# Kernel tuning notes

Measured on AMD Instinct MI355X. Metric: run time of the kernel, lower is better.

## Reference

```python
import jax, jax.numpy as jnp
import numpy as np

JACCARD_THRESH = 0.5
NEGPOS_RATIO = 3
VAR = (0.1, 0.2)


def point_form(p):
    # center-size (cx,cy,w,h) -> corner (xmin,ymin,xmax,ymax)
    return jnp.concatenate([p[:, :2] - p[:, 2:] / 2, p[:, :2] + p[:, 2:] / 2], axis=1)


def jaccard(a, b):
    # a: [No,4] corner boxes, b: [Np,4] corner boxes -> IoU [No,Np]
    lt = jnp.maximum(a[:, None, :2], b[None, :, :2])
    rb = jnp.minimum(a[:, None, 2:], b[None, :, 2:])
    wh = jnp.clip(rb - lt, 0.0)
    inter = wh[..., 0] * wh[..., 1]
    area_a = ((a[:, 2] - a[:, 0]) * (a[:, 3] - a[:, 1]))[:, None]
    area_b = ((b[:, 2] - b[:, 0]) * (b[:, 3] - b[:, 1]))[None, :]
    return inter / (area_a + area_b - inter)


def encode(matched, priors):
    # matched: [Np,4] corner GT, priors: [Np,4] center-size
    g_cxcy = ((matched[:, :2] + matched[:, 2:]) / 2 - priors[:, :2]) / (VAR[0] * priors[:, 2:])
    g_wh = jnp.log((matched[:, 2:] - matched[:, :2]) / priors[:, 2:]) / VAR[1]
    return jnp.concatenate([g_cxcy, g_wh], axis=1)


def match_one(truths, labels, priors):
    # truths: [No,4], labels: [No], priors: [Np,4] center-size
    overlaps = jaccard(truths, point_form(priors))          # [No,Np]
    best_prior_idx = jnp.argmax(overlaps, axis=1)           # [No]
    best_truth_overlap = jnp.max(overlaps, axis=0)          # [Np]
    best_truth_idx = jnp.argmax(overlaps, axis=0)           # [Np]
    # each GT keeps its best prior (overlap forced to 2)
    best_truth_overlap = best_truth_overlap.at[best_prior_idx].set(2.0)
    best_truth_idx = best_truth_idx.at[best_prior_idx].set(jnp.arange(truths.shape[0]))
    matched = truths[best_truth_idx]                        # [Np,4]
    conf = labels[best_truth_idx].astype(jnp.int32) + 1     # background = 0
    conf = jnp.where(best_truth_overlap < JACCARD_THRESH, 0, conf)
    return encode(matched, priors), conf


def reference(loc_data, conf_data, dbox_list, targets):
    num_batch, num_dbox, num_classes = conf_data.shape
    truths = targets[:, :, :4]
    labels = targets[:, :, 4]
    loc_t, conf_t = jax.vmap(match_one, in_axes=(0, 0, None))(truths, labels, dbox_list)
    pos_mask = conf_t > 0                                   # [B,Np]
    # localization loss: SmoothL1 (beta=1), summed over positive dboxes
    diff = loc_data - loc_t
    ad = jnp.abs(diff)
    sl1 = jnp.where(ad < 1.0, 0.5 * diff * diff, ad - 0.5)
    loss_l = jnp.sum(sl1 * pos_mask[..., None].astype(sl1.dtype))
    # per-dbox cross entropy
    logp = jax.nn.log_softmax(conf_data, axis=-1)
    ce = -jnp.take_along_axis(logp, conf_t[..., None], axis=-1)[..., 0]  # [B,Np]
    # hard negative mining: rank (descending) of pos-zeroed CE via double argsort
    loss_c_hnm = jnp.where(pos_mask, 0.0, ce)
    loss_idx = jnp.argsort(-loss_c_hnm, axis=1)
    idx_rank = jnp.argsort(loss_idx, axis=1)
    num_pos = jnp.sum(pos_mask, axis=1, keepdims=True)      # [B,1]
    num_neg = jnp.minimum(num_pos * NEGPOS_RATIO, num_dbox)
    neg_mask = idx_rank < num_neg
    sel = jnp.logical_or(pos_mask, neg_mask)
    loss_c = jnp.sum(jnp.where(sel, ce, 0.0))
    N = jnp.sum(num_pos).astype(loss_l.dtype)
    return loss_l / N, loss_c / N


def setup_inputs() -> dict:
    key = jax.random.key(0)
    ks = jax.random.split(key, 7)
    B, Np, C, No = 128, 8732, 21, 16
    loc_data = jax.random.normal(ks[0], (B, Np, 4), dtype=jnp.float32) * 0.1
    conf_data = jax.random.normal(ks[1], (B, Np, C), dtype=jnp.float32)
    # default boxes in center-size form, w/h strictly positive
    cxcy = jax.random.uniform(ks[2], (Np, 2), minval=0.05, maxval=0.95)
    wh = jax.random.uniform(ks[3], (Np, 2), minval=0.05, maxval=0.5)
    dbox_list = jnp.concatenate([cxcy, wh], axis=1).astype(jnp.float32)
    # ground truth: valid corner-form boxes + class label in [0,20)
    gcxcy = jax.random.uniform(ks[4], (B, No, 2), minval=0.2, maxval=0.8)
    gwh = jax.random.uniform(ks[5], (B, No, 2), minval=0.05, maxval=0.3)
    boxes = jnp.concatenate([gcxcy - gwh / 2, gcxcy + gwh / 2], axis=-1)
    lab = jax.random.randint(ks[6], (B, No, 1), 0, C - 1).astype(jnp.float32)
    targets = jnp.concatenate([boxes, lab], axis=-1).astype(jnp.float32)
    return {"loc_data": loc_data, "conf_data": conf_data, "dbox_list": dbox_list, "targets": targets}
```

## Files before the change

kernel.cpp:

```cpp
#include <hip/hip_runtime.h>
#include <stdint.h>

#define TPB 256
#define PPT 4
#define SELTPB 1024
#define SELWAVES (SELTPB / 64)
#define MAXNO 64
#define NMB 16

__device__ __forceinline__ float sl1f(float d) {
    float ad = fabsf(d);
    return ad < 1.0f ? 0.5f * d * d : ad - 0.5f;
}

__device__ __forceinline__ float iou_pair(float tx1, float ty1, float tx2, float ty2, float ta,
                                          float px1, float py1, float px2, float py2, float pa) {
    float ltx = fmaxf(tx1, px1), lty = fmaxf(ty1, py1);
    float rbx = fminf(tx2, px2), rby = fminf(ty2, py2);
    float wx = fmaxf(rbx - ltx, 0.0f), wy = fmaxf(rby - lty, 0.0f);
    float inter = wx * wy;
    return inter / ((ta + pa) - inter);
}

template <int NO>
__global__ __launch_bounds__(256) void match_partial_kernel(
    const float* __restrict__ dbox, const float* __restrict__ targets,
    unsigned long long* __restrict__ pkeys, int Np, int No) {
    int b = blockIdx.y, mb = blockIdx.x;
    int tid = threadIdx.x;
    __shared__ float s_t[NO][5];
    __shared__ unsigned long long s_k[4][NO];
    if (tid < No) {
        const float* tr = targets + ((size_t)b * No + tid) * 5;
        float x1 = tr[0], y1 = tr[1], x2 = tr[2], y2 = tr[3];
        s_t[tid][0] = x1; s_t[tid][1] = y1; s_t[tid][2] = x2; s_t[tid][3] = y2;
        s_t[tid][4] = (x2 - x1) * (y2 - y1);
    }
    __syncthreads();
    int clen = (Np + NMB - 1) / NMB;
    int start = mb * clen;
    int end = start + clen;
    if (end > Np) end = Np;
    unsigned long long key[NO];
#pragma unroll
    for (int t = 0; t < NO; ++t) key[t] = 0ull;
    for (int p = start + tid; p < end; p += 256) {
        float4 pr = *reinterpret_cast<const float4*>(dbox + (size_t)p * 4);
        float px1 = pr.x - pr.z * 0.5f, py1 = pr.y - pr.w * 0.5f;
        float px2 = pr.x + pr.z * 0.5f, py2 = pr.y + pr.w * 0.5f;
        float pa = (px2 - px1) * (py2 - py1);
        unsigned lowp = 0xFFFFFFFFu - (unsigned)p;
#pragma unroll
        for (int t = 0; t < NO; ++t) {
            float iou = iou_pair(s_t[t][0], s_t[t][1], s_t[t][2], s_t[t][3], s_t[t][4],
                                 px1, py1, px2, py2, pa);
            unsigned long long k =
                (((unsigned long long)__float_as_uint(iou)) << 32) | (unsigned long long)lowp;
            if (k > key[t]) key[t] = k;
        }
    }
    int lane = tid & 63, wv = tid >> 6;
#pragma unroll
    for (int t = 0; t < NO; ++t) {
        unsigned long long k = key[t];
        for (int off = 32; off; off >>= 1) {
            unsigned long long o = __shfl_down(k, off);
            if (o > k) k = o;
        }
        if (lane == 0) s_k[wv][t] = k;
    }
    __syncthreads();
    if (tid < No) {
        unsigned long long m = s_k[0][tid];
#pragma unroll
        for (int w = 1; w < 4; ++w)
            if (s_k[w][tid] > m) m = s_k[w][tid];
        pkeys[((size_t)b * NMB + mb) * No + tid] = m;
    }
}

__global__ __launch_bounds__(64) void combine_kernel(
    const unsigned long long* __restrict__ pkeys, const float* __restrict__ targets,
    float* __restrict__ tmeta, int No) {
    int b = blockIdx.x, t = threadIdx.x;
    if (t >= No) return;
    unsigned long long k = pkeys[((size_t)b * NMB + 0) * No + t];
    for (int m = 1; m < NMB; ++m) {
        unsigned long long kk = pkeys[((size_t)b * NMB + m) * No + t];
        if (kk > k) k = kk;
    }
    const float* tr = targets + ((size_t)b * No + t) * 5;
    float x1 = tr[0], y1 = tr[1], x2 = tr[2], y2 = tr[3];
    float* tm = tmeta + ((size_t)b * MAXNO + t) * 8;
    tm[0] = x1; tm[1] = y1; tm[2] = x2; tm[3] = y2;
    tm[4] = (x2 - x1) * (y2 - y1);
    tm[5] = tr[4];
    tm[6] = __uint_as_float(0xFFFFFFFFu - (unsigned)(k & 0xFFFFFFFFull));
    tm[7] = 0.0f;
}

template <int CC, int TNO>
__global__ __launch_bounds__(TPB) void main_kernel(
    const float* __restrict__ loc, const float* __restrict__ conf,
    const float* __restrict__ dbox, const float* __restrict__ tmeta,
    float* __restrict__ v, float* __restrict__ part_l, float* __restrict__ part_c,
    int* __restrict__ part_n, int Np, int C, int No, int nchunk) {
    __shared__ float s_tb[MAXNO][5];
    __shared__ float s_red1[4];
    __shared__ float s_red2[4];
    __shared__ int s_redi[4];
    int b = blockIdx.y, chunk = blockIdx.x, tid = threadIdx.x;
    int pbase = chunk * (TPB * PPT);
    if (tid < No) {
        const float* tm = tmeta + ((size_t)b * MAXNO + tid) * 8;
        s_tb[tid][0] = tm[0]; s_tb[tid][1] = tm[1];
        s_tb[tid][2] = tm[2]; s_tb[tid][3] = tm[3];
        s_tb[tid][4] = tm[5];
    }
    __syncthreads();

    float lossl = 0.0f, posce = 0.0f;
    int npos = 0;
#pragma unroll 1
    for (int pp = 0; pp < PPT; ++pp) {
        int p = pbase + pp * TPB + tid;
        if (p >= Np) break;
        float4 pr = *reinterpret_cast<const float4*>(dbox + (size_t)p * 4);
        float px1 = pr.x - pr.z * 0.5f, py1 = pr.y - pr.w * 0.5f;
        float px2 = pr.x + pr.z * 0.5f, py2 = pr.y + pr.w * 0.5f;
        float pa = (px2 - px1) * (py2 - py1);
        float bov = -1.0f;
        int bidx = 0;
        int ovt = -1;
        if (TNO > 0) {
#pragma unroll
            for (int t = 0; t < TNO; ++t) {
                const float* tm = tmeta + ((size_t)b * MAXNO + t) * 8;
                float iou = iou_pair(tm[0], tm[1], tm[2], tm[3], tm[4],
                                     px1, py1, px2, py2, pa);
                if (iou > bov) { bov = iou; bidx = t; }
                if (__float_as_uint(tm[6]) == (unsigned)p) ovt = t;
            }
        } else {
            for (int t = 0; t < No; ++t) {
                const float* tm = tmeta + ((size_t)b * MAXNO + t) * 8;
                float iou = iou_pair(tm[0], tm[1], tm[2], tm[3], tm[4],
                                     px1, py1, px2, py2, pa);
                if (iou > bov) { bov = iou; bidx = t; }
                if (__float_as_uint(tm[6]) == (unsigned)p) ovt = t;
            }
        }
        if (ovt >= 0) { bidx = ovt; bov = 2.0f; }
        int ct = (bov < 0.5f) ? 0 : ((int)s_tb[bidx][4] + 1);
        float ce;
        const float* crow = conf + ((size_t)b * Np + p) * C;
        if (CC > 0) {
            float fr[CC > 0 ? CC : 1];
            float mx = -1e30f, fc = 0.0f;
#pragma unroll
            for (int j = 0; j < CC; ++j) {
                float x = crow[j];
                fr[j] = x;
                mx = fmaxf(mx, x);
                fc = (j == ct) ? x : fc;
            }
            float s = 0.0f;
#pragma unroll
            for (int j = 0; j < CC; ++j) s += __expf(fr[j] - mx);
            ce = __logf(s) + mx - fc;
        } else {
            float mx = crow[0];
            for (int j = 1; j < C; ++j) mx = fmaxf(mx, crow[j]);
            float s = 0.0f;
            for (int j = 0; j < C; ++j) s += __expf(crow[j] - mx);
            ce = __logf(s) + mx - crow[ct];
        }
        bool pos = ct > 0;
        v[(size_t)b * Np + p] = pos ? 0.0f : ce;
        if (pos) {
            posce += ce;
            npos += 1;
            float mx1 = s_tb[bidx][0], my1 = s_tb[bidx][1];
            float mx2 = s_tb[bidx][2], my2 = s_tb[bidx][3];
            float gcx = ((mx1 + mx2) * 0.5f - pr.x) / (0.1f * pr.z);
            float gcy = ((my1 + my2) * 0.5f - pr.y) / (0.1f * pr.w);
            float gw = __logf((mx2 - mx1) / pr.z) / 0.2f;
            float gh = __logf((my2 - my1) / pr.w) / 0.2f;
            float4 l4 = *reinterpret_cast<const float4*>(loc + ((size_t)b * Np + p) * 4);
            lossl += sl1f(l4.x - gcx) + sl1f(l4.y - gcy) + sl1f(l4.z - gw) + sl1f(l4.w - gh);
        }
    }
    float a1 = lossl, a2 = posce;
    int ni = npos;
    for (int off = 32; off; off >>= 1) {
        a1 += __shfl_down(a1, off);
        a2 += __shfl_down(a2, off);
        ni += __shfl_down(ni, off);
    }
    if ((tid & 63) == 0) {
        s_red1[tid >> 6] = a1;
        s_red2[tid >> 6] = a2;
        s_redi[tid >> 6] = ni;
    }
    __syncthreads();
    if (tid == 0) {
        part_l[(size_t)b * nchunk + chunk] = s_red1[0] + s_red1[1] + s_red1[2] + s_red1[3];
        part_c[(size_t)b * nchunk + chunk] = s_red2[0] + s_red2[1] + s_red2[2] + s_red2[3];
        part_n[(size_t)b * nchunk + chunk] = s_redi[0] + s_redi[1] + s_redi[2] + s_redi[3];
    }
}

__global__ __launch_bounds__(SELTPB) void select_kernel(
    const float* __restrict__ v, const float* __restrict__ pl,
    const float* __restrict__ pc, const int* __restrict__ pn,
    float* __restrict__ row_res, int Np, int nchunk, int negpos) {
    int b = blockIdx.x, tid = threadIdx.x;
    int lane = tid & 63, wv = tid >> 6;
    extern __shared__ unsigned sv[];
    __shared__ unsigned whist[SELWAVES][256];
    __shared__ float s_f[SELWAVES];
    __shared__ int s_dig, s_acc;
    __shared__ float s_lossl, s_posce;
    __shared__ int s_np;

    if (wv == 0) {
        float a = 0.0f, c = 0.0f;
        int n = 0;
        for (int i = lane; i < nchunk; i += 64) {
            a += pl[(size_t)b * nchunk + i];
            c += pc[(size_t)b * nchunk + i];
            n += pn[(size_t)b * nchunk + i];
        }
        for (int off = 32; off; off >>= 1) {
            a += __shfl_down(a, off);
            c += __shfl_down(c, off);
            n += __shfl_down(n, off);
        }
        if (lane == 0) { s_lossl = a; s_posce = c; s_np = n; }
    }
    {
        const float4* v4 = reinterpret_cast<const float4*>(v + (size_t)b * Np);
        int n4 = Np >> 2;
        for (int i = tid; i < n4; i += SELTPB) {
            float4 f = v4[i];
            uint4 u;
            u.x = __float_as_uint(f.x); u.y = __float_as_uint(f.y);
            u.z = __float_as_uint(f.z); u.w = __float_as_uint(f.w);
            *reinterpret_cast<uint4*>(&sv[i << 2]) = u;
        }
        for (int i = (n4 << 2) + tid; i < Np; i += SELTPB)
            sv[i] = __float_as_uint(v[(size_t)b * Np + i]);
    }
    __syncthreads();
    int npos = s_np;
    int K = npos * negpos;
    if (K > Np) K = Np;
    float lossc = s_posce;
    if (K > 0) {
        unsigned prefix = 0;
        int Krem = K;
        for (int shift = 24; shift >= 0; shift -= 8) {
            for (int i = tid; i < SELWAVES * 256; i += SELTPB)
                (&whist[0][0])[i] = 0;
            __syncthreads();
            for (int i = tid; i < Np; i += SELTPB) {
                unsigned u = sv[i];
                bool match = (shift == 24) || ((u >> (shift + 8)) == (prefix >> (shift + 8)));
                if (match) atomicAdd(&whist[wv][(u >> shift) & 0xFFu], 1u);
            }
            __syncthreads();
            if (wv == 0) {
                unsigned t0 = 0, t1 = 0, t2 = 0, t3 = 0;
#pragma unroll
                for (int w = 0; w < SELWAVES; ++w) {
                    t0 += whist[w][4 * lane + 0];
                    t1 += whist[w][4 * lane + 1];
                    t2 += whist[w][4 * lane + 2];
                    t3 += whist[w][4 * lane + 3];
                }
                unsigned s = t0 + t1 + t2 + t3;
                unsigned run = s;
                for (int off = 1; off < 64; off <<= 1) {
                    unsigned o = __shfl_down(run, off);
                    if (lane + off < 64) run += o;
                }
                unsigned hi = run - s;
                unsigned S3 = hi + t3, S2 = S3 + t2, S1 = S2 + t1, S0 = S1 + t0;
                unsigned kr = (unsigned)Krem;
                if (S3 >= kr && hi < kr) { s_dig = 4 * lane + 3; s_acc = (int)hi; }
                else if (S2 >= kr && S3 < kr) { s_dig = 4 * lane + 2; s_acc = (int)S3; }
                else if (S1 >= kr && S2 < kr) { s_dig = 4 * lane + 1; s_acc = (int)S2; }
                else if (S0 >= kr && S1 < kr) { s_dig = 4 * lane + 0; s_acc = (int)S1; }
            }
            __syncthreads();
            prefix |= ((unsigned)s_dig) << shift;
            Krem -= s_acc;
        }
        float sum_gt = 0.0f;
        for (int i = tid; i < Np; i += SELTPB) {
            unsigned u = sv[i];
            if (u > prefix) sum_gt += __uint_as_float(u);
        }
        for (int off = 32; off; off >>= 1) sum_gt += __shfl_down(sum_gt, off);
        if (lane == 0) s_f[wv] = sum_gt;
        __syncthreads();
        if (tid == 0) {
            float t = 0.0f;
            for (int w = 0; w < SELWAVES; ++w) t += s_f[w];
            lossc += t + (float)Krem * __uint_as_float(prefix);
        }
    }
    if (tid == 0) {
        row_res[(size_t)b * 3 + 0] = s_lossl;
        row_res[(size_t)b * 3 + 1] = lossc;
        row_res[(size_t)b * 3 + 2] = (float)npos;
    }
}

__global__ __launch_bounds__(TPB) void finalize_kernel(
    const float* __restrict__ row_res, float* __restrict__ out, int B) {
    int tid = threadIdx.x;
    float l = 0, c = 0, n = 0;
    for (int i = tid; i < B; i += TPB) {
        l += row_res[(size_t)i * 3 + 0];
        c += row_res[(size_t)i * 3 + 1];
        n += row_res[(size_t)i * 3 + 2];
    }
    __shared__ float sl[4], sc[4], sn[4];
    for (int off = 32; off; off >>= 1) {
        l += __shfl_down(l, off);
        c += __shfl_down(c, off);
        n += __shfl_down(n, off);
    }
    int lane = tid & 63, w = tid >> 6;
    if (lane == 0) { sl[w] = l; sc[w] = c; sn[w] = n; }
    __syncthreads();
    if (tid == 0) {
        l = sl[0] + sl[1] + sl[2] + sl[3];
        c = sc[0] + sc[1] + sc[2] + sc[3];
        n = sn[0] + sn[1] + sn[2] + sn[3];
        out[0] = l / n;
        out[1] = c / n;
    }
}

extern "C" void kernel_launch(void* const* d_in, const int* in_sizes, int n_in,
                              void* d_out, int out_size, void* d_ws, size_t ws_size,
                              hipStream_t stream) {
    const float* loc = (const float*)d_in[0];
    const float* conf = (const float*)d_in[1];
    const float* dbox = (const float*)d_in[2];
    const float* targets = (const float*)d_in[3];

    int Np = in_sizes[2] / 4;
    int B = in_sizes[0] / (Np * 4);
    int C = in_sizes[1] / (B * Np);
    int No = in_sizes[3] / (B * 5);
    int nchunk = (Np + TPB * PPT - 1) / (TPB * PPT);

    char* w = (char*)d_ws;
    unsigned long long* pkeys = (unsigned long long*)w;
    w += (size_t)B * NMB * No * sizeof(unsigned long long);
    float* tmeta = (float*)w;
    w += (size_t)B * MAXNO * 8 * sizeof(float);
    float* v = (float*)w;
    w += (size_t)B * Np * sizeof(float);
    float* part_l = (float*)w;
    w += (size_t)B * nchunk * sizeof(float);
    float* part_c = (float*)w;
    w += (size_t)B * nchunk * sizeof(float);
    int* part_n = (int*)w;
    w += (size_t)B * nchunk * sizeof(int);
    float* row_res = (float*)w;

    dim3 mgrid(NMB, B);
    if (No == 16)
        match_partial_kernel<16><<<mgrid, 256, 0, stream>>>(dbox, targets, pkeys, Np, No);
    else
        match_partial_kernel<MAXNO><<<mgrid, 256, 0, stream>>>(dbox, targets, pkeys, Np, No);

    combine_kernel<<<B, 64, 0, stream>>>(pkeys, targets, tmeta, No);

    dim3 grid(nchunk, B);
    if (C == 21 && No == 16)
        main_kernel<21, 16><<<grid, TPB, 0, stream>>>(loc, conf, dbox, tmeta,
                                                      v, part_l, part_c, part_n, Np, C, No, nchunk);
    else
        main_kernel<0, 0><<<grid, TPB, 0, stream>>>(loc, conf, dbox, tmeta,
                                                    v, part_l, part_c, part_n, Np, C, No, nchunk);
    select_kernel<<<B, SELTPB, (size_t)Np * sizeof(float), stream>>>(v, part_l, part_c, part_n,
                                                                     row_res, Np, nchunk, 3);
    finalize_kernel<<<1, TPB, 0, stream>>>(row_res, (float*)d_out, B);
}
```

Measured before the change: 84.24 us.

## Split log-sum-exp into separate coalesced LDS-staged kernel before matching

```diff
diff --git a/kernel.cpp b/kernel.cpp
--- a/kernel.cpp
+++ b/kernel.cpp
@@ -2,7 +2,7 @@
 #include <stdint.h>
 
 #define TPB 256
-#define PPT 4
+#define PPT 2
 #define SELTPB 1024
 #define SELWAVES (SELTPB / 64)
 #define MAXNO 64
@@ -99,8 +99,55 @@
     tm[7] = 0.0f;
 }
 
-template <int CC, int TNO>
-__global__ __launch_bounds__(TPB) void main_kernel(
+template <int CC>
+__global__ __launch_bounds__(TPB) void ce_kernel(
+    const float* __restrict__ conf, float* __restrict__ v, int Np, int C) {
+    extern __shared__ float s_conf[];
+    int b = blockIdx.y, chunk = blockIdx.x, tid = threadIdx.x;
+    int pbase = chunk * TPB;
+    int cnt = Np - pbase;
+    if (cnt > TPB) cnt = TPB;
+    const float* cbase = conf + ((size_t)b * Np + (size_t)pbase) * C;
+    {
+        int ntot = cnt * C;
+        int nv4 = ntot >> 2;
+        const float4* c4 = reinterpret_cast<const float4*>(cbase);
+        float4* s4 = reinterpret_cast<float4*>(s_conf);
+        for (int i = tid; i < nv4; i += TPB) s4[i] = c4[i];
+        for (int i = (nv4 << 2) + tid; i < ntot; i += TPB) s_conf[i] = cbase[i];
+    }
+    __syncthreads();
+    int p = pbase + tid;
+    if (tid < cnt) {
+        float lse;
+        if (CC > 0) {
+            const float* crow = s_conf + tid * CC;
+            float fr[CC > 0 ? CC : 1];
+            float mx = -1e30f;
+#pragma unroll
+            for (int j = 0; j < CC; ++j) {
+                float x = crow[j];
+                fr[j] = x;
+                mx = fmaxf(mx, x);
+            }
+            float s = 0.0f;
+#pragma unroll
+            for (int j = 0; j < CC; ++j) s += __expf(fr[j] - mx);
+            lse = __logf(s) + mx;
+        } else {
+            const float* crow = s_conf + (size_t)tid * C;
+            float mx = crow[0];
+            for (int j = 1; j < C; ++j) mx = fmaxf(mx, crow[j]);
+            float s = 0.0f;
+            for (int j = 0; j < C; ++j) s += __expf(crow[j] - mx);
+            lse = __logf(s) + mx;
+        }
+        v[(size_t)b * Np + p] = lse;
+    }
+}
+
+template <int TNO>
+__global__ __launch_bounds__(TPB) void match_loss_kernel(
     const float* __restrict__ loc, const float* __restrict__ conf,
     const float* __restrict__ dbox, const float* __restrict__ tmeta,
     float* __restrict__ v, float* __restrict__ part_l, float* __restrict__ part_c,
@@ -152,29 +199,8 @@
         }
         if (ovt >= 0) { bidx = ovt; bov = 2.0f; }
         int ct = (bov < 0.5f) ? 0 : ((int)s_tb[bidx][4] + 1);
-        float ce;
-        const float* crow = conf + ((size_t)b * Np + p) * C;
-        if (CC > 0) {
-            float fr[CC > 0 ? CC : 1];
-            float mx = -1e30f, fc = 0.0f;
-#pragma unroll
-            for (int j = 0; j < CC; ++j) {
-                float x = crow[j];
-                fr[j] = x;
-                mx = fmaxf(mx, x);
-                fc = (j == ct) ? x : fc;
-            }
-            float s = 0.0f;
-#pragma unroll
-            for (int j = 0; j < CC; ++j) s += __expf(fr[j] - mx);
-            ce = __logf(s) + mx - fc;
-        } else {
-            float mx = crow[0];
-            for (int j = 1; j < C; ++j) mx = fmaxf(mx, crow[j]);
-            float s = 0.0f;
-            for (int j = 0; j < C; ++j) s += __expf(crow[j] - mx);
-            ce = __logf(s) + mx - crow[ct];
-        }
+        float xct = conf[((size_t)b * Np + p) * C + ct];
+        float ce = v[(size_t)b * Np + p] - xct;
         bool pos = ct > 0;
         v[(size_t)b * Np + p] = pos ? 0.0f : ce;
         if (pos) {
@@ -356,6 +382,7 @@
     int B = in_sizes[0] / (Np * 4);
     int C = in_sizes[1] / (B * Np);
     int No = in_sizes[3] / (B * 5);
+    int nchunk_ce = (Np + TPB - 1) / TPB;
     int nchunk = (Np + TPB * PPT - 1) / (TPB * PPT);
 
     char* w = (char*)d_ws;
@@ -381,13 +408,20 @@
 
     combine_kernel<<<B, 64, 0, stream>>>(pkeys, targets, tmeta, No);
 
+    dim3 cegrid(nchunk_ce, B);
+    size_t lds_ce = (size_t)TPB * C * sizeof(float);
+    if (C == 21)
+        ce_kernel<21><<<cegrid, TPB, lds_ce, stream>>>(conf, v, Np, C);
+    else
+        ce_kernel<0><<<cegrid, TPB, lds_ce, stream>>>(conf, v, Np, C);
+
     dim3 grid(nchunk, B);
-    if (C == 21 && No == 16)
-        main_kernel<21, 16><<<grid, TPB, 0, stream>>>(loc, conf, dbox, tmeta,
-                                                      v, part_l, part_c, part_n, Np, C, No, nchunk);
+    if (No == 16)
+        match_loss_kernel<16><<<grid, TPB, 0, stream>>>(loc, conf, dbox, tmeta,
+                                                        v, part_l, part_c, part_n, Np, C, No, nchunk);
     else
-        main_kernel<0, 0><<<grid, TPB, 0, stream>>>(loc, conf, dbox, tmeta,
-                                                    v, part_l, part_c, part_n, Np, C, No, nchunk);
+        match_loss_kernel<0><<<grid, TPB, 0, stream>>>(loc, conf, dbox, tmeta,
+                                                       v, part_l, part_c, part_n, Np, C, No, nchunk);
     select_kernel<<<B, SELTPB, (size_t)Np * sizeof(float), stream>>>(v, part_l, part_c, part_n,
                                                                      row_res, Np, nchunk, 3);
     finalize_kernel<<<1, TPB, 0, stream>>>(row_res, (float*)d_out, B);
```

Result: slower. 92.11 us (+9.3%).

## Fold combine step into main kernel and batch IoU over priors per thread

Applied to the files above, without the earlier changes.

```diff
diff --git a/kernel.cpp b/kernel.cpp
--- a/kernel.cpp
+++ b/kernel.cpp
@@ -79,95 +79,99 @@
     }
 }
 
-__global__ __launch_bounds__(64) void combine_kernel(
-    const unsigned long long* __restrict__ pkeys, const float* __restrict__ targets,
-    float* __restrict__ tmeta, int No) {
-    int b = blockIdx.x, t = threadIdx.x;
-    if (t >= No) return;
-    unsigned long long k = pkeys[((size_t)b * NMB + 0) * No + t];
-    for (int m = 1; m < NMB; ++m) {
-        unsigned long long kk = pkeys[((size_t)b * NMB + m) * No + t];
-        if (kk > k) k = kk;
-    }
-    const float* tr = targets + ((size_t)b * No + t) * 5;
-    float x1 = tr[0], y1 = tr[1], x2 = tr[2], y2 = tr[3];
-    float* tm = tmeta + ((size_t)b * MAXNO + t) * 8;
-    tm[0] = x1; tm[1] = y1; tm[2] = x2; tm[3] = y2;
-    tm[4] = (x2 - x1) * (y2 - y1);
-    tm[5] = tr[4];
-    tm[6] = __uint_as_float(0xFFFFFFFFu - (unsigned)(k & 0xFFFFFFFFull));
-    tm[7] = 0.0f;
-}
-
 template <int CC, int TNO>
 __global__ __launch_bounds__(TPB) void main_kernel(
     const float* __restrict__ loc, const float* __restrict__ conf,
-    const float* __restrict__ dbox, const float* __restrict__ tmeta,
+    const float* __restrict__ dbox, const float* __restrict__ targets,
+    const unsigned long long* __restrict__ pkeys,
     float* __restrict__ v, float* __restrict__ part_l, float* __restrict__ part_c,
     int* __restrict__ part_n, int Np, int C, int No, int nchunk) {
-    __shared__ float s_tb[MAXNO][5];
+    __shared__ float s_tb[(TNO > 0 ? TNO : MAXNO)][6];
+    __shared__ unsigned s_ovr[(TNO > 0 ? TNO : MAXNO)];
     __shared__ float s_red1[4];
     __shared__ float s_red2[4];
     __shared__ int s_redi[4];
     int b = blockIdx.y, chunk = blockIdx.x, tid = threadIdx.x;
     int pbase = chunk * (TPB * PPT);
     if (tid < No) {
-        const float* tm = tmeta + ((size_t)b * MAXNO + tid) * 8;
-        s_tb[tid][0] = tm[0]; s_tb[tid][1] = tm[1];
-        s_tb[tid][2] = tm[2]; s_tb[tid][3] = tm[3];
-        s_tb[tid][4] = tm[5];
-    }
-    __syncthreads();
+        const float* tr = targets + ((size_t)b * No + tid) * 5;
+        float x1 = tr[0], y1 = tr[1], x2 = tr[2], y2 = tr[3];
+        s_tb[tid][0] = x1; s_tb[tid][1] = y1; s_tb[tid][2] = x2; s_tb[tid][3] = y2;
+        s_tb[tid][4] = (x2 - x1) * (y2 - y1);
+        s_tb[tid][5] = tr[4];
+        unsigned long long k = pkeys[((size_t)b * NMB + 0) * No + tid];
+#pragma unroll
+        for (int m = 1; m < NMB; ++m) {
+            unsigned long long kk = pkeys[((size_t)b * NMB + m) * No + tid];
+            if (kk > k) k = kk;
+        }
+        s_ovr[tid] = 0xFFFFFFFFu - (unsigned)(k & 0xFFFFFFFFull);
+    }
+    __syncthreads();
+
+    float px1[PPT], py1[PPT], px2[PPT], py2[PPT], pa[PPT];
+    float bov[PPT];
+    int bidx[PPT], ovt[PPT];
+    bool vld[PPT];
+#pragma unroll
+    for (int pp = 0; pp < PPT; ++pp) {
+        int p = pbase + pp * TPB + tid;
+        vld[pp] = p < Np;
+        bov[pp] = -1.0f; bidx[pp] = 0; ovt[pp] = -1;
+        if (vld[pp]) {
+            float4 pr = *reinterpret_cast<const float4*>(dbox + (size_t)p * 4);
+            px1[pp] = pr.x - pr.z * 0.5f; py1[pp] = pr.y - pr.w * 0.5f;
+            px2[pp] = pr.x + pr.z * 0.5f; py2[pp] = pr.y + pr.w * 0.5f;
+            pa[pp] = (px2[pp] - px1[pp]) * (py2[pp] - py1[pp]);
+        } else {
+            px1[pp] = 0; py1[pp] = 0; px2[pp] = 0; py2[pp] = 0; pa[pp] = 0;
+        }
+    }
+    int nt = (TNO > 0) ? TNO : No;
+    for (int t = 0; t < nt; ++t) {
+        float tx1 = s_tb[t][0], ty1 = s_tb[t][1], tx2 = s_tb[t][2], ty2 = s_tb[t][3];
+        float ta = s_tb[t][4];
+        unsigned ov = s_ovr[t];
+#pragma unroll
+        for (int pp = 0; pp < PPT; ++pp) {
+            int p = pbase + pp * TPB + tid;
+            float iou = iou_pair(tx1, ty1, tx2, ty2, ta,
+                                 px1[pp], py1[pp], px2[pp], py2[pp], pa[pp]);
+            if (iou > bov[pp]) { bov[pp] = iou; bidx[pp] = t; }
+            if (ov == (unsigned)p) ovt[pp] = t;
+        }
+    }
 
     float lossl = 0.0f, posce = 0.0f;
     int npos = 0;
-#pragma unroll 1
+#pragma unroll
     for (int pp = 0; pp < PPT; ++pp) {
+        if (!vld[pp]) continue;
         int p = pbase + pp * TPB + tid;
-        if (p >= Np) break;
-        float4 pr = *reinterpret_cast<const float4*>(dbox + (size_t)p * 4);
-        float px1 = pr.x - pr.z * 0.5f, py1 = pr.y - pr.w * 0.5f;
-        float px2 = pr.x + pr.z * 0.5f, py2 = pr.y + pr.w * 0.5f;
-        float pa = (px2 - px1) * (py2 - py1);
-        float bov = -1.0f;
-        int bidx = 0;
-        int ovt = -1;
-        if (TNO > 0) {
-#pragma unroll
-            for (int t = 0; t < TNO; ++t) {
-                const float* tm = tmeta + ((size_t)b * MAXNO + t) * 8;
-                float iou = iou_pair(tm[0], tm[1], tm[2], tm[3], tm[4],
-                                     px1, py1, px2, py2, pa);
-                if (iou > bov) { bov = iou; bidx = t; }
-                if (__float_as_uint(tm[6]) == (unsigned)p) ovt = t;
+        int bi = bidx[pp];
+        float bv = bov[pp];
+        if (ovt[pp] >= 0) { bi = ovt[pp]; bv = 2.0f; }
+        int ct = (bv < 0.5f) ? 0 : ((int)s_tb[bi][5] + 1);
+        const float* crow = conf + ((size_t)b * Np + p) * C;
+        float ce;
+        if (CC > 0) {
+            float x[CC > 0 ? CC : 1];
+#pragma unroll
+            for (int j = 0; j < CC; ++j) x[j] = __builtin_nontemporal_load(&crow[j]);
+            float mx = x[0], fc = x[0];
+#pragma unroll
+            for (int j = 1; j < CC; ++j) {
+                mx = fmaxf(mx, x[j]);
+                fc = (j == ct) ? x[j] : fc;
             }
-        } else {
-            for (int t = 0; t < No; ++t) {
-                const float* tm = tmeta + ((size_t)b * MAXNO + t) * 8;
-                float iou = iou_pair(tm[0], tm[1], tm[2], tm[3], tm[4],
-                                     px1, py1, px2, py2, pa);
-                if (iou > bov) { bov = iou; bidx = t; }
-                if (__float_as_uint(tm[6]) == (unsigned)p) ovt = t;
+            float s0 = 0.0f, s1 = 0.0f;
+#pragma unroll
+            for (int j = 0; j + 1 < CC; j += 2) {
+                s0 += __expf(x[j] - mx);
+                s1 += __expf(x[j + 1] - mx);
             }
-        }
-        if (ovt >= 0) { bidx = ovt; bov = 2.0f; }
-        int ct = (bov < 0.5f) ? 0 : ((int)s_tb[bidx][4] + 1);
-        float ce;
-        const float* crow = conf + ((size_t)b * Np + p) * C;
-        if (CC > 0) {
-            float fr[CC > 0 ? CC : 1];
-            float mx = -1e30f, fc = 0.0f;
-#pragma unroll
-            for (int j = 0; j < CC; ++j) {
-                float x = crow[j];
-                fr[j] = x;
-                mx = fmaxf(mx, x);
-                fc = (j == ct) ? x : fc;
-            }
-            float s = 0.0f;
-#pragma unroll
-            for (int j = 0; j < CC; ++j) s += __expf(fr[j] - mx);
-            ce = __logf(s) + mx - fc;
+            if (CC & 1) s0 += __expf(x[CC - 1] - mx);
+            ce = __logf(s0 + s1) + mx - fc;
         } else {
             float mx = crow[0];
             for (int j = 1; j < C; ++j) mx = fmaxf(mx, crow[j]);
@@ -180,12 +184,14 @@
         if (pos) {
             posce += ce;
             npos += 1;
-            float mx1 = s_tb[bidx][0], my1 = s_tb[bidx][1];
-            float mx2 = s_tb[bidx][2], my2 = s_tb[bidx][3];
-            float gcx = ((mx1 + mx2) * 0.5f - pr.x) / (0.1f * pr.z);
-            float gcy = ((my1 + my2) * 0.5f - pr.y) / (0.1f * pr.w);
-            float gw = __logf((mx2 - mx1) / pr.z) / 0.2f;
-            float gh = __logf((my2 - my1) / pr.w) / 0.2f;
+            float mx1 = s_tb[bi][0], my1 = s_tb[bi][1];
+            float mx2 = s_tb[bi][2], my2 = s_tb[bi][3];
+            float pcx = (px1[pp] + px2[pp]) * 0.5f, pcy = (py1[pp] + py2[pp]) * 0.5f;
+            float pw = px2[pp] - px1[pp], ph = py2[pp] - py1[pp];
+            float gcx = ((mx1 + mx2) * 0.5f - pcx) / (0.1f * pw);
+            float gcy = ((my1 + my2) * 0.5f - pcy) / (0.1f * ph);
+            float gw = __logf((mx2 - mx1) / pw) / 0.2f;
+            float gh = __logf((my2 - my1) / ph) / 0.2f;
             float4 l4 = *reinterpret_cast<const float4*>(loc + ((size_t)b * Np + p) * 4);
             lossl += sl1f(l4.x - gcx) + sl1f(l4.y - gcy) + sl1f(l4.z - gw) + sl1f(l4.w - gh);
         }
@@ -361,8 +367,6 @@
     char* w = (char*)d_ws;
     unsigned long long* pkeys = (unsigned long long*)w;
     w += (size_t)B * NMB * No * sizeof(unsigned long long);
-    float* tmeta = (float*)w;
-    w += (size_t)B * MAXNO * 8 * sizeof(float);
     float* v = (float*)w;
     w += (size_t)B * Np * sizeof(float);
     float* part_l = (float*)w;
@@ -379,14 +383,12 @@
     else
         match_partial_kernel<MAXNO><<<mgrid, 256, 0, stream>>>(dbox, targets, pkeys, Np, No);
 
-    combine_kernel<<<B, 64, 0, stream>>>(pkeys, targets, tmeta, No);
-
     dim3 grid(nchunk, B);
     if (C == 21 && No == 16)
-        main_kernel<21, 16><<<grid, TPB, 0, stream>>>(loc, conf, dbox, tmeta,
+        main_kernel<21, 16><<<grid, TPB, 0, stream>>>(loc, conf, dbox, targets, pkeys,
                                                       v, part_l, part_c, part_n, Np, C, No, nchunk);
     else
-        main_kernel<0, 0><<<grid, TPB, 0, stream>>>(loc, conf, dbox, tmeta,
+        main_kernel<0, 0><<<grid, TPB, 0, stream>>>(loc, conf, dbox, targets, pkeys,
                                                     v, part_l, part_c, part_n, Np, C, No, nchunk);
     select_kernel<<<B, SELTPB, (size_t)Np * sizeof(float), stream>>>(v, part_l, part_c, part_n,
                                                                      row_res, Np, nchunk, 3);
```

Measured after the change: 102.3 us. 1.21x slower.
